# Kernel tuning notes

Hardware: AMD Instinct MI355X
Metric: run time of the kernel (lower is better)

The kernel has to match this reference:

```python
import jax, jax.numpy as jnp
import numpy as np
from jax import lax

D_MODEL = 1024
H = 16
D_K = D_MODEL // H
B = 2
S = 1024


def _conv3x3(x, w, b):
    # x: [B, C_in, S, S], w: [C_out, C_in, 3, 3], b: [C_out]; SAME padding=1
    y = lax.conv_general_dilated(x, w, window_strides=(1, 1),
                                 padding=((1, 1), (1, 1)),
                                 dimension_numbers=("NCHW", "OIHW", "NCHW"))
    return y + b[None, :, None, None]


def setup_inputs() -> dict:
    key = jax.random.key(0)
    ks = jax.random.split(key, 12)
    q = jax.random.normal(ks[0], (B, S, D_MODEL), dtype=jnp.float32)
    k = jax.random.normal(ks[1], (B, S, D_MODEL), dtype=jnp.float32)
    v = jax.random.normal(ks[2], (B, S, D_MODEL), dtype=jnp.float32)
    mask = jax.random.randint(ks[3], (B, S), 0, 2, dtype=jnp.int32)
    prev = jax.random.normal(ks[4], (B, H, S, S), dtype=jnp.float32)
    sc = 1.0 / np.sqrt(D_MODEL)
    Wq = jax.random.normal(ks[5], (D_MODEL, D_MODEL), dtype=jnp.float32) * sc
    Wk = jax.random.normal(ks[6], (D_MODEL, D_MODEL), dtype=jnp.float32) * sc
    Wv = jax.random.normal(ks[7], (D_MODEL, D_MODEL), dtype=jnp.float32) * sc
    Wo = jax.random.normal(ks[8], (D_MODEL, D_MODEL), dtype=jnp.float32) * sc
    csc = 1.0 / np.sqrt(H * 9)
    Wt = jax.random.normal(ks[9], (H, H, 3, 3), dtype=jnp.float32) * csc
    bt = jnp.zeros((H,), dtype=jnp.float32)
    Wa = jax.random.normal(ks[10], (H, 2 * H, 3, 3), dtype=jnp.float32) * csc
    ba = jnp.zeros((H,), dtype=jnp.float32)
    return {"q": q, "k": k, "v": v, "mask": mask,
            "previous_attention_scores": prev,
            "Wq": Wq, "Wk": Wk, "Wv": Wv, "Wo": Wo,
            "Wt": Wt, "bt": bt, "Wa": Wa, "ba": ba}


def reference(q, k, v, mask, previous_attention_scores,
              Wq, Wk, Wv, Wo, Wt, bt, Wa, ba):
    # Linear projections (torch Linear: x @ W.T), reshape to [B, H, S, D_K]
    def split_heads(x):
        return x.reshape(B, S, H, D_K).transpose(0, 2, 1, 3)
    query = split_heads(q @ Wq.T)
    key_ = split_heads(k @ Wk.T)
    value = split_heads(v @ Wv.T)

    # Raw (unscaled) scores: [B, H, S, S]
    M = jnp.einsum("bhsd,bhtd->bhst", query, key_)
    # Transmit conv on previous layer's attention scores (heads = channels)
    Mt = _conv3x3(previous_attention_scores, Wt, bt)
    # Aggregate conv over concatenated [M, Mt]: 2H -> H channels
    Ma = _conv3x3(jnp.concatenate((M, Mt), axis=1), Wa, ba)
    # NOTE: original scales by sqrt(d_model), not sqrt(d_k)
    A = jax.nn.softmax(Ma / jnp.sqrt(jnp.float32(D_MODEL)), axis=-1)
    # NOTE: original applies masked_fill(-1e9) AFTER softmax (faithful)
    A = jnp.where(mask[:, None, None, :] == 0, jnp.float32(-1e9), A)

    ctx = jnp.einsum("bhst,bhtd->bhsd", A, value)  # [B, H, S, D_K]
    ctx = ctx.transpose(0, 2, 1, 3).reshape(B, S, H * D_K)
    out = ctx @ Wo.T
    return out, A
```

## Files before the change

kernel.cpp:

```cpp
#include <hip/hip_runtime.h>

#define B_  2
#define S_  1024
#define H_  16
#define DK_ 64
#define D_  1024

static const size_t BSD  = (size_t)B_ * S_ * D_;
static const size_t BHSS = (size_t)B_ * H_ * S_ * S_;

typedef __attribute__((ext_vector_type(8))) short bf16x8;
typedef __attribute__((ext_vector_type(4))) float floatx4;

__device__ __forceinline__ unsigned short f2bf(float f) {
  unsigned u = __builtin_bit_cast(unsigned, f);
  unsigned r = (u + 0x7FFFu + ((u >> 16) & 1u)) >> 16;
  return (unsigned short)r;
}

__global__ __launch_bounds__(256) void cvt_bf16_kernel(
    const float* __restrict__ src, unsigned short* __restrict__ dst, int n4) {
  int i = (blockIdx.x << 8) + threadIdx.x;
  if (i >= n4) return;
  float4 v = ((const float4*)src)[i];
  ushort4 o;
  o.x = f2bf(v.x); o.y = f2bf(v.y); o.z = f2bf(v.z); o.w = f2bf(v.w);
  ((ushort4*)dst)[i] = o;
}

__global__ __launch_bounds__(256) void gemm_bf16_nt_kernel(
    const unsigned short* __restrict__ A, const unsigned short* __restrict__ Bw,
    void* __restrict__ Cout, int K, int Mcols, int bf16_out,
    const float* __restrict__ corr) {
  __shared__ short As[64 * 40];
  __shared__ short Bs[64 * 40];
  int tid = threadIdx.x;
  int lane = tid & 63, w = tid >> 6;
  int quad = lane >> 4, xn = lane & 15;
  int row0 = blockIdx.y << 6, col0 = blockIdx.x << 6;
  int rw = w & 1, cw = w >> 1;
  int srow = tid >> 2, sk = (tid & 3) << 3;
  const unsigned short* Ap = A + (size_t)(row0 + srow) * K + sk;
  const unsigned short* Bp = Bw + (size_t)(col0 + srow) * K + sk;
  floatx4 acc[2][2] = {};
  for (int k0 = 0; k0 < K; k0 += 32) {
    uint4 av = *(const uint4*)(Ap + k0);
    uint4 bv = *(const uint4*)(Bp + k0);
    *(uint4*)&As[srow * 40 + sk] = av;
    *(uint4*)&Bs[srow * 40 + sk] = bv;
    __syncthreads();
    bf16x8 af[2], bf[2];
#pragma unroll
    for (int rt = 0; rt < 2; ++rt)
      af[rt] = *(const bf16x8*)&As[(rw * 32 + rt * 16 + xn) * 40 + quad * 8];
#pragma unroll
    for (int ct = 0; ct < 2; ++ct)
      bf[ct] = *(const bf16x8*)&Bs[(cw * 32 + ct * 16 + xn) * 40 + quad * 8];
#pragma unroll
    for (int rt = 0; rt < 2; ++rt)
#pragma unroll
      for (int ct = 0; ct < 2; ++ct)
        acc[rt][ct] = __builtin_amdgcn_mfma_f32_16x16x32_bf16(
            af[rt], bf[ct], acc[rt][ct], 0, 0, 0);
    __syncthreads();
  }
#pragma unroll
  for (int rt = 0; rt < 2; ++rt)
#pragma unroll
    for (int ct = 0; ct < 2; ++ct) {
      int colg = col0 + cw * 32 + ct * 16 + xn;
#pragma unroll
      for (int r = 0; r < 4; ++r) {
        int rowg = row0 + rw * 32 + rt * 16 + quad * 4 + r;
        if (bf16_out)
          ((unsigned short*)Cout)[(size_t)rowg * Mcols + colg] = f2bf(acc[rt][ct][r]);
        else {
          float v = acc[rt][ct][r];
          if (corr) v += corr[((rowg >> 10) << 10) + colg];
          ((float*)Cout)[(size_t)rowg * Mcols + colg] = v;
        }
      }
    }
}

__global__ __launch_bounds__(256) void scores_mfma_kernel(
    const unsigned short* __restrict__ Q, const unsigned short* __restrict__ Km,
    unsigned short* __restrict__ Mo) {
  __shared__ short Qs[128 * 72];
  __shared__ short Ks[64 * 72];
  int z = blockIdx.z, b = z >> 4, h = z & 15;
  int col0 = blockIdx.x << 6, row0 = blockIdx.y << 7;
  int tid = threadIdx.x;
  int lane = tid & 63, w = tid >> 6;
  int quad = lane >> 4, xn = lane & 15;
  const unsigned short* Qb = Q + (size_t)b * S_ * D_ + h * DK_;
  const unsigned short* Kb = Km + (size_t)b * S_ * D_ + h * DK_;
  for (int idx = tid; idx < 1024; idx += 256) {
    int r = idx >> 3, k8 = (idx & 7) << 3;
    uint4 v = *(const uint4*)&Qb[(size_t)(row0 + r) * D_ + k8];
    *(uint4*)&Qs[r * 72 + k8] = v;
  }
  for (int idx = tid; idx < 512; idx += 256) {
    int r = idx >> 3, k8 = (idx & 7) << 3;
    uint4 v = *(const uint4*)&Kb[(size_t)(col0 + r) * D_ + k8];
    *(uint4*)&Ks[r * 72 + k8] = v;
  }
  __syncthreads();
  floatx4 acc[2][4] = {};
#pragma unroll
  for (int ks = 0; ks < 2; ++ks) {
    bf16x8 af[2], bf[4];
#pragma unroll
    for (int rt = 0; rt < 2; ++rt)
      af[rt] = *(const bf16x8*)&Qs[(w * 32 + rt * 16 + xn) * 72 + ks * 32 + quad * 8];
#pragma unroll
    for (int ct = 0; ct < 4; ++ct)
      bf[ct] = *(const bf16x8*)&Ks[(ct * 16 + xn) * 72 + ks * 32 + quad * 8];
#pragma unroll
    for (int rt = 0; rt < 2; ++rt)
#pragma unroll
      for (int ct = 0; ct < 4; ++ct)
        acc[rt][ct] = __builtin_amdgcn_mfma_f32_16x16x32_bf16(
            af[rt], bf[ct], acc[rt][ct], 0, 0, 0);
  }
  unsigned short* Mb = Mo + (size_t)z * S_ * S_;
#pragma unroll
  for (int rt = 0; rt < 2; ++rt)
#pragma unroll
    for (int ct = 0; ct < 4; ++ct) {
      int t = col0 + ct * 16 + xn;
#pragma unroll
      for (int r = 0; r < 4; ++r) {
        int s = row0 + w * 32 + rt * 16 + quad * 4 + r;
        Mb[(size_t)s * S_ + t] = f2bf(acc[rt][ct][r]);
      }
    }
}

__global__ __launch_bounds__(256) void repack16b_kernel(
    const unsigned short* __restrict__ src, unsigned short* __restrict__ dst) {
  int x = (blockIdx.x << 8) + threadIdx.x;
  int y = blockIdx.y, b = blockIdx.z;
  const unsigned short* sp = src + ((size_t)b * 16 * S_ + y) * S_ + x;
  unsigned short out[16];
#pragma unroll
  for (int c = 0; c < 16; ++c) out[c] = sp[(size_t)c << 20];
  unsigned short* dp = dst + (((size_t)b * S_ + y) * S_ + x) * 16;
  unsigned wds[8];
#pragma unroll
  for (int i = 0; i < 8; ++i)
    wds[i] = (unsigned)out[2 * i] | ((unsigned)out[2 * i + 1] << 16);
  uint4 v0 = {wds[0], wds[1], wds[2], wds[3]};
  uint4 v1 = {wds[4], wds[5], wds[6], wds[7]};
  *(uint4*)dp = v0;
  *((uint4*)dp + 1) = v1;
}

__global__ __launch_bounds__(256) void repack16_kernel(
    const float* __restrict__ src, unsigned short* __restrict__ dst) {
  int x = (blockIdx.x << 8) + threadIdx.x;
  int y = blockIdx.y, b = blockIdx.z;
  const float* sp = src + ((size_t)b * 16 * S_ + y) * S_ + x;
  unsigned short out[16];
#pragma unroll
  for (int c = 0; c < 16; ++c) out[c] = f2bf(sp[(size_t)c << 20]);
  unsigned short* dp = dst + (((size_t)b * S_ + y) * S_ + x) * 16;
  unsigned wds[8];
#pragma unroll
  for (int i = 0; i < 8; ++i)
    wds[i] = (unsigned)out[2 * i] | ((unsigned)out[2 * i + 1] << 16);
  uint4 v0 = {wds[0], wds[1], wds[2], wds[3]};
  uint4 v1 = {wds[4], wds[5], wds[6], wds[7]};
  *(uint4*)dp = v0;
  *((uint4*)dp + 1) = v1;
}

__global__ __launch_bounds__(256) void conv_t_mfma_kernel(
    const unsigned short* __restrict__ prevT, const float* __restrict__ Wt,
    const float* __restrict__ bt, unsigned short* __restrict__ Mtbf) {
  __shared__ short Xs[10 * 66 * 24];
  int b = blockIdx.z;
  int x0 = blockIdx.x << 6, y0 = blockIdx.y << 3;
  int tid = threadIdx.x;
  int lane = tid & 63, w = tid >> 6;
  int quad = lane >> 4, xn = lane & 15;

  for (int idx = tid; idx < 1320; idx += 256) {
    int y = idx / 132;
    int r = idx - y * 132;
    int px = r >> 1, half = r & 1;
    int gy = y0 + y - 1, gx = x0 + px - 1;
    uint4 val = {0u, 0u, 0u, 0u};
    if ((unsigned)gy < (unsigned)S_ && (unsigned)gx < (unsigned)S_) {
      const unsigned short* sp =
          prevT + (((size_t)b * S_ + gy) * S_ + gx) * 16 + half * 8;
      val = *(const uint4*)sp;
    }
    *(uint4*)&Xs[(y * 66 + px) * 24 + half * 8] = val;
  }

  int m = xn;
  bf16x8 afr[5];
#pragma unroll
  for (int p = 0; p < 5; ++p) {
#pragma unroll
    for (int j = 0; j < 8; ++j) {
      int k = quad * 8 + j;
      int t = 2 * p + (k >> 4);
      float wv = 0.f;
      if (t < 9) wv = Wt[(m * 16 + (k & 15)) * 9 + t];
      afr[p][j] = (short)f2bf(wv);
    }
  }
  int tdy[5], tdx[5];
#pragma unroll
  for (int p = 0; p < 5; ++p) {
    int t = 2 * p + (quad >> 1);
    if (t > 8) t = 8;
    tdy[p] = t / 3;
    tdx[p] = t - tdy[p] * 3;
  }
  float btl[4];
#pragma unroll
  for (int r = 0; r < 4; ++r) btl[r] = bt[quad * 4 + r];

  __syncthreads();

#pragma unroll
  for (int ry = 0; ry < 2; ++ry) {
    int yl = w * 2 + ry;
    int y = y0 + yl;
#pragma unroll
    for (int seg = 0; seg < 4; ++seg) {
      floatx4 acc = {0.f, 0.f, 0.f, 0.f};
#pragma unroll
      for (int p = 0; p < 5; ++p) {
        const short* bp =
            &Xs[((yl + tdy[p]) * 66 + seg * 16 + xn + tdx[p]) * 24 + (quad & 1) * 8];
        bf16x8 bfr = *(const bf16x8*)bp;
        acc = __builtin_amdgcn_mfma_f32_16x16x32_bf16(afr[p], bfr, acc, 0, 0, 0);
      }
      ushort4 pk;
      pk.x = f2bf(acc[0] + btl[0]);
      pk.y = f2bf(acc[1] + btl[1]);
      pk.z = f2bf(acc[2] + btl[2]);
      pk.w = f2bf(acc[3] + btl[3]);
      int gx = x0 + seg * 16 + xn;
      *(ushort4*)&Mtbf[(((size_t)b * S_ + y) * S_ + gx) * 16 + quad * 4] = pk;
    }
  }
}

__global__ __launch_bounds__(256) void conv_a_softmax_kernel(
    const unsigned short* __restrict__ Mbf, const unsigned short* __restrict__ Mtbf,
    const float* __restrict__ Wa, const float* __restrict__ ba,
    const int* __restrict__ mask,
    float* __restrict__ Aout, unsigned short* __restrict__ P0) {
  __shared__ __attribute__((aligned(16))) short Xs[4 * 3 * 34 * 40];
  __shared__ float redm[4][4][4];
  __shared__ float reds[4][4][4];
  int y = ((blockIdx.x & 7) << 7) + (blockIdx.x >> 3);
  int b = blockIdx.y;
  int tid = threadIdx.x;
  int lane = tid & 63, w = tid >> 6;
  int quad = lane >> 4, xn = lane & 15;

  bf16x8 afr[9];
#pragma unroll
  for (int t = 0; t < 9; ++t)
#pragma unroll
    for (int j = 0; j < 8; ++j)
      afr[t][j] = (short)f2bf(Wa[(xn * 32 + quad * 8 + j) * 9 + t]);
  float bal[4];
#pragma unroll
  for (int r = 0; r < 4; ++r) bal[r] = ba[quad * 4 + r];

  short* XsW = &Xs[w * (3 * 34 * 40)];

  int px4 = lane >> 2, part = lane & 3;
  const unsigned short* rowp[3];
  int vy[3];
#pragma unroll
  for (int ry = 0; ry < 3; ++ry) {
    int gy = y + ry - 1;
    vy[ry] = ((unsigned)gy < (unsigned)S_) ? 1 : 0;
    int gyc = vy[ry] ? gy : 0;
    const unsigned short* base = (part < 2) ? Mbf : Mtbf;
    rowp[ry] = base + ((size_t)b * S_ + gyc) * (S_ * 16) + (part & 1) * 8;
  }

  floatx4 acc[8][2] = {};
#pragma unroll
  for (int ci = 0; ci < 8; ++ci) {
    int x0 = (ci << 7) + (w << 5);
#pragma unroll
    for (int ry = 0; ry < 3; ++ry) {
#pragma unroll
      for (int g = 0; g < 3; ++g) {
        if (g < 2 || px4 < 2) {
          int px = (g << 4) + px4;
          int gx = x0 + px - 1;
          uint4 val = {0u, 0u, 0u, 0u};
          if (vy[ry] && (unsigned)gx < (unsigned)S_)
            val = *(const uint4*)(rowp[ry] + (size_t)gx * 16);
          *(uint4*)&XsW[(ry * 34 + px) * 40 + part * 8] = val;
        }
      }
    }
    __builtin_amdgcn_wave_barrier();
#pragma unroll
    for (int sub = 0; sub < 2; ++sub) {
      int sp = (sub << 4) + xn;
      floatx4 a = acc[ci][sub];
#pragma unroll
      for (int t = 0; t < 9; ++t) {
        const int dy = t / 3, dx = t - (t / 3) * 3;
        bf16x8 bfr = *(const bf16x8*)&XsW[(dy * 34 + sp + dx) * 40 + quad * 8];
        a = __builtin_amdgcn_mfma_f32_16x16x32_bf16(afr[t], bfr, a, 0, 0, 0);
      }
      acc[ci][sub] = a;
    }
    __builtin_amdgcn_wave_barrier();
  }

  const float sc = 1.0f / 32.0f;
  float mx[4] = {-3.4e38f, -3.4e38f, -3.4e38f, -3.4e38f};
#pragma unroll
  for (int ci = 0; ci < 8; ++ci)
#pragma unroll
    for (int sub = 0; sub < 2; ++sub)
#pragma unroll
      for (int r = 0; r < 4; ++r) {
        float v = (acc[ci][sub][r] + bal[r]) * sc;
        acc[ci][sub][r] = v;
        mx[r] = fmaxf(mx[r], v);
      }
#pragma unroll
  for (int r = 0; r < 4; ++r) {
    mx[r] = fmaxf(mx[r], __shfl_xor(mx[r], 1));
    mx[r] = fmaxf(mx[r], __shfl_xor(mx[r], 2));
    mx[r] = fmaxf(mx[r], __shfl_xor(mx[r], 4));
    mx[r] = fmaxf(mx[r], __shfl_xor(mx[r], 8));
  }
  if (xn == 0) {
#pragma unroll
    for (int r = 0; r < 4; ++r) redm[w][quad][r] = mx[r];
  }
  __syncthreads();
  float fm[4];
#pragma unroll
  for (int r = 0; r < 4; ++r)
    fm[r] = fmaxf(fmaxf(redm[0][quad][r], redm[1][quad][r]),
                  fmaxf(redm[2][quad][r], redm[3][quad][r]));
  float sm[4] = {0.f, 0.f, 0.f, 0.f};
#pragma unroll
  for (int ci = 0; ci < 8; ++ci)
#pragma unroll
    for (int sub = 0; sub < 2; ++sub)
#pragma unroll
      for (int r = 0; r < 4; ++r) {
        float e = __expf(acc[ci][sub][r] - fm[r]);
        acc[ci][sub][r] = e;
        sm[r] += e;
      }
#pragma unroll
  for (int r = 0; r < 4; ++r) {
    sm[r] += __shfl_xor(sm[r], 1);
    sm[r] += __shfl_xor(sm[r], 2);
    sm[r] += __shfl_xor(sm[r], 4);
    sm[r] += __shfl_xor(sm[r], 8);
  }
  if (xn == 0) {
#pragma unroll
    for (int r = 0; r < 4; ++r) reds[w][quad][r] = sm[r];
  }
  __syncthreads();
  float inv[4];
#pragma unroll
  for (int r = 0; r < 4; ++r)
    inv[r] = 1.0f / (reds[0][quad][r] + reds[1][quad][r] +
                     reds[2][quad][r] + reds[3][quad][r]);

  const int* mb = mask + b * S_;
#pragma unroll
  for (int ci = 0; ci < 8; ++ci)
#pragma unroll
    for (int sub = 0; sub < 2; ++sub) {
      int gx = (ci << 7) + (w << 5) + (sub << 4) + xn;
      int mk = mb[gx];
#pragma unroll
      for (int r = 0; r < 4; ++r) {
        int mo = quad * 4 + r;
        size_t oidx = (((size_t)(b * 16 + mo)) << 20) + ((size_t)y << 10) + gx;
        float p = acc[ci][sub][r] * inv[r];
        Aout[oidx] = mk ? p : -1e9f;
        P0[oidx]  = mk ? f2bf(p) : (unsigned short)0;
      }
    }
}

__global__ __launch_bounds__(256) void vtrans_kernel(
    const float* __restrict__ V, unsigned short* __restrict__ Vt) {
  __shared__ unsigned short Ls[64][68];
  int z = blockIdx.y, b = z >> 4, h = z & 15;
  int t0 = blockIdx.x << 6;
  int tid = threadIdx.x;
  for (int idx = tid; idx < 1024; idx += 256) {
    int t = idx >> 4, d = (idx & 15) << 2;
    float4 v4 = *(const float4*)&V[((size_t)b * S_ + t0 + t) * D_ + h * 64 + d];
    ushort4 u;
    u.x = f2bf(v4.x); u.y = f2bf(v4.y); u.z = f2bf(v4.z); u.w = f2bf(v4.w);
    *(ushort4*)&Ls[t][d] = u;
  }
  __syncthreads();
  for (int idx = tid; idx < 1024; idx += 256) {
    int d = idx >> 4, tc = (idx & 15) << 2;
    ushort4 u;
    u.x = Ls[tc + 0][d]; u.y = Ls[tc + 1][d];
    u.z = Ls[tc + 2][d]; u.w = Ls[tc + 3][d];
    *(ushort4*)&Vt[((size_t)(h * 64 + d)) * 2048 + (size_t)b * S_ + t0 + tc] = u;
  }
}

__global__ __launch_bounds__(256) void colsum_part_kernel(
    const float* __restrict__ V, const int* __restrict__ mask,
    float* __restrict__ cs_part) {
  int b = blockIdx.z, c = blockIdx.y;
  int d = (blockIdx.x << 8) + threadIdx.x;
  const int* mb = mask + b * S_ + c * 32;
  const float* vp = V + ((size_t)b * S_ + c * 32) * D_ + d;
  float s = 0.f;
#pragma unroll
  for (int i = 0; i < 32; ++i) {
    float vv = vp[(size_t)i * D_];
    if (mb[i] == 0) s += vv;
  }
  cs_part[((size_t)b * 32 + c) * D_ + d] = s;
}

__global__ __launch_bounds__(256) void colsum_reduce_kernel(
    const float* __restrict__ cs_part, float* __restrict__ cs) {
  int i = (blockIdx.x << 8) + threadIdx.x;
  int b = i >> 10, d = i & 1023;
  const float* pp = cs_part + ((size_t)b * 32) * D_ + d;
  float s = 0.f;
#pragma unroll
  for (int c = 0; c < 32; ++c) s += pp[(size_t)c * D_];
  cs[i] = s;
}

__global__ __launch_bounds__(256) void corr_kernel(
    const float* __restrict__ cs, const float* __restrict__ Wo,
    float* __restrict__ corr) {
  int b = blockIdx.y;
  int j = (blockIdx.x << 6) + (threadIdx.x >> 2);
  int part = threadIdx.x & 3;
  const float* c = cs + b * D_ + part * 256;
  const float* wr = Wo + (size_t)j * D_ + part * 256;
  float s = 0.f;
  for (int i = 0; i < 256; i += 4) {
    float4 w4 = *(const float4*)&wr[i];
    float4 c4 = *(const float4*)&c[i];
    s = fmaf(w4.x, c4.x, s); s = fmaf(w4.y, c4.y, s);
    s = fmaf(w4.z, c4.z, s); s = fmaf(w4.w, c4.w, s);
  }
  s += __shfl_xor(s, 1);
  s += __shfl_xor(s, 2);
  if (part == 0) corr[b * D_ + j] = -1e9f * s;
}

__global__ __launch_bounds__(256) void ctx_mfma_kernel(
    const unsigned short* __restrict__ P0, const unsigned short* __restrict__ Vt,
    unsigned short* __restrict__ Cbf) {
  __shared__ __attribute__((aligned(16))) short Ps[64 * 72];
  __shared__ __attribute__((aligned(16))) short Vs[64 * 72];
  int z = blockIdx.y, b = z >> 4, h = z & 15;
  int row0 = blockIdx.x << 6;
  int tid = threadIdx.x, lane = tid & 63, w = tid >> 6;
  int quad = lane >> 4, xn = lane & 15;
  const unsigned short* Pb = P0 + (size_t)z * S_ * S_ + (size_t)row0 * S_;
  const unsigned short* Vb = Vt + ((size_t)h * 64) * 2048 + (size_t)b * S_;
  floatx4 acc[4] = {};
  for (int k0 = 0; k0 < S_; k0 += 64) {
    for (int idx = tid; idx < 512; idx += 256) {
      int r = idx >> 3, c = (idx & 7) << 3;
      *(uint4*)&Ps[r * 72 + c] = *(const uint4*)&Pb[(size_t)r * S_ + k0 + c];
    }
    for (int idx = tid; idx < 512; idx += 256) {
      int r = idx >> 3, c = (idx & 7) << 3;
      *(uint4*)&Vs[r * 72 + c] = *(const uint4*)&Vb[(size_t)r * 2048 + k0 + c];
    }
    __syncthreads();
#pragma unroll
    for (int ks = 0; ks < 2; ++ks) {
      bf16x8 af = *(const bf16x8*)&Ps[(w * 16 + xn) * 72 + ks * 32 + quad * 8];
#pragma unroll
      for (int ct = 0; ct < 4; ++ct) {
        bf16x8 bfv = *(const bf16x8*)&Vs[(ct * 16 + xn) * 72 + ks * 32 + quad * 8];
        acc[ct] = __builtin_amdgcn_mfma_f32_16x16x32_bf16(af, bfv, acc[ct], 0, 0, 0);
      }
    }
    __syncthreads();
  }
  unsigned short* Co = Cbf + ((size_t)b * S_) * D_ + h * 64;
#pragma unroll
  for (int ct = 0; ct < 4; ++ct)
#pragma unroll
    for (int r = 0; r < 4; ++r) {
      int s = row0 + w * 16 + quad * 4 + r;
      Co[(size_t)s * D_ + ct * 16 + xn] = f2bf(acc[ct][r]);
    }
}

extern "C" void kernel_launch(void* const* d_in, const int* in_sizes, int n_in,
                              void* d_out, int out_size, void* d_ws, size_t ws_size,
                              hipStream_t stream) {
  const float* q    = (const float*)d_in[0];
  const float* k    = (const float*)d_in[1];
  const float* v    = (const float*)d_in[2];
  const int*   mask = (const int*)d_in[3];
  const float* prev = (const float*)d_in[4];
  const float* Wq   = (const float*)d_in[5];
  const float* Wk   = (const float*)d_in[6];
  const float* Wv   = (const float*)d_in[7];
  const float* Wo   = (const float*)d_in[8];
  const float* Wt   = (const float*)d_in[9];
  const float* bt   = (const float*)d_in[10];
  const float* Wa   = (const float*)d_in[11];
  const float* ba   = (const float*)d_in[12];

  float* out0 = (float*)d_out;
  float* Aout = out0 + BSD;

  char* wsp = (char*)d_ws;
  unsigned short* X1   = (unsigned short*)wsp; wsp += BSD * 2;
  unsigned short* W1   = (unsigned short*)wsp; wsp += (size_t)D_ * D_ * 2;
  unsigned short* Qb   = (unsigned short*)wsp; wsp += BSD * 2;
  unsigned short* Kb   = (unsigned short*)wsp; wsp += BSD * 2;
  float* Vb            = (float*)wsp;          wsp += BSD * 4;
  unsigned short* Vtb  = (unsigned short*)wsp; wsp += BSD * 2;
  unsigned short* ctx1 = (unsigned short*)wsp; wsp += BSD * 2;
  float* cs            = (float*)wsp;          wsp += (size_t)B_ * D_ * 4;
  float* corrb         = (float*)wsp;          wsp += (size_t)B_ * D_ * 4;
  float* cs_part       = (float*)wsp;          wsp += (size_t)B_ * 32 * D_ * 4;
  unsigned short* Mp   = (unsigned short*)wsp; wsp += BHSS * 2;
  unsigned short* Mbf  = (unsigned short*)wsp; wsp += BHSS * 2;
  unsigned short* Mtbf = (unsigned short*)wsp; wsp += BHSS * 2;
  unsigned short* prevT = Mp;
  unsigned short* P0    = Mp;

  dim3 blk(256);
  int n4x = (int)(BSD / 4);
  int n4w = (D_ * D_) / 4;
  dim3 gX((n4x + 255) / 256), gW((n4w + 255) / 256);
  dim3 gProjB(D_ / 64, (B_ * S_) / 64);

  hipLaunchKernelGGL(cvt_bf16_kernel, gW, blk, 0, stream, Wq, W1, n4w);
  hipLaunchKernelGGL(cvt_bf16_kernel, gX, blk, 0, stream, q, X1, n4x);
  hipLaunchKernelGGL(gemm_bf16_nt_kernel, gProjB, blk, 0, stream, X1, W1,
                     (void*)Qb, D_, D_, 1, (const float*)nullptr);
  hipLaunchKernelGGL(cvt_bf16_kernel, gW, blk, 0, stream, Wk, W1, n4w);
  hipLaunchKernelGGL(cvt_bf16_kernel, gX, blk, 0, stream, k, X1, n4x);
  hipLaunchKernelGGL(gemm_bf16_nt_kernel, gProjB, blk, 0, stream, X1, W1,
                     (void*)Kb, D_, D_, 1, (const float*)nullptr);
  hipLaunchKernelGGL(cvt_bf16_kernel, gW, blk, 0, stream, Wv, W1, n4w);
  hipLaunchKernelGGL(cvt_bf16_kernel, gX, blk, 0, stream, v, X1, n4x);
  hipLaunchKernelGGL(gemm_bf16_nt_kernel, gProjB, blk, 0, stream, X1, W1,
                     (void*)Vb, D_, D_, 0, (const float*)nullptr);
  hipLaunchKernelGGL(cvt_bf16_kernel, gW, blk, 0, stream, Wo, W1, n4w);

  hipLaunchKernelGGL(vtrans_kernel, dim3(S_ / 64, B_ * H_), blk, 0, stream, Vb, Vtb);
  hipLaunchKernelGGL(colsum_part_kernel, dim3(D_ / 256, 32, B_), blk, 0, stream,
                     Vb, mask, cs_part);
  hipLaunchKernelGGL(colsum_reduce_kernel, dim3((B_ * D_) / 256), blk, 0, stream,
                     cs_part, cs);
  hipLaunchKernelGGL(corr_kernel, dim3(D_ / 64, B_), blk, 0, stream, cs, Wo, corrb);

  dim3 gSc(S_ / 64, S_ / 128, B_ * H_);
  hipLaunchKernelGGL(scores_mfma_kernel, gSc, blk, 0, stream, Qb, Kb, Mp);

  dim3 gRep(S_ / 256, S_, B_);
  hipLaunchKernelGGL(repack16b_kernel, gRep, blk, 0, stream, Mp, Mbf);

  hipLaunchKernelGGL(repack16_kernel, gRep, blk, 0, stream, prev, prevT);

  dim3 gConv(S_ / 64, S_ / 8, B_);
  hipLaunchKernelGGL(conv_t_mfma_kernel, gConv, blk, 0, stream, prevT, Wt, bt, Mtbf);

  hipLaunchKernelGGL(conv_a_softmax_kernel, dim3(S_, B_), blk, 0, stream,
                     Mbf, Mtbf, Wa, ba, mask, Aout, P0);

  hipLaunchKernelGGL(ctx_mfma_kernel, dim3(S_ / 64, B_ * H_), blk, 0, stream,
                     P0, Vtb, ctx1);

  dim3 gProj(D_ / 64, (B_ * S_) / 64);
  hipLaunchKernelGGL(gemm_bf16_nt_kernel, gProj, blk, 0, stream, ctx1, W1,
                     (void*)out0, D_, D_, 0, (const float*)corrb);
}
```

Baseline: 675.9 us.

## Prefetch next conv tile into registers and repack LDS layout per channel-quad

In the aggregate-conv+softmax kernel, global loads for the next 32-column chunk are issued into registers before the MFMA work on the current chunk, software-pipelining global latency behind compute. The LDS staging layout changes from pixel-major with 40-short padding to a [row][channel-quad][pixel] layout with 8-short rows. This shrinks LDS per block and changes bank access patterns. Load index math is precomputed once per thread. The cost is extra registers for seven uint4 prefetch buffers plus precomputed pointers, which may reduce occupancy.

```diff
diff --git a/kernel.cpp b/kernel.cpp
--- a/kernel.cpp
+++ b/kernel.cpp
@@ -256,7 +256,7 @@
     const float* __restrict__ Wa, const float* __restrict__ ba,
     const int* __restrict__ mask,
     float* __restrict__ Aout, unsigned short* __restrict__ P0) {
-  __shared__ __attribute__((aligned(16))) short Xs[4 * 3 * 34 * 40];
+  __shared__ __attribute__((aligned(16))) short Xs[4 * 3264];
   __shared__ float redm[4][4][4];
   __shared__ float reds[4][4][4];
   int y = ((blockIdx.x & 7) << 7) + (blockIdx.x >> 3);
@@ -275,39 +275,63 @@
 #pragma unroll
   for (int r = 0; r < 4; ++r) bal[r] = ba[quad * 4 + r];
 
-  short* XsW = &Xs[w * (3 * 34 * 40)];
-
-  int px4 = lane >> 2, part = lane & 3;
-  const unsigned short* rowp[3];
-  int vy[3];
-#pragma unroll
-  for (int ry = 0; ry < 3; ++ry) {
+  short* XsW = &Xs[w * 3264];
+
+  const unsigned short* s_base[7];
+  int s_pxo[7], s_lds[7], s_vy[7];
+#pragma unroll
+  for (int it = 0; it < 7; ++it) {
+    int s = it * 64 + lane;
+    int ry = (s >= 272) ? 2 : ((s >= 136) ? 1 : 0);
+    int rem = s - ry * 136;
+    int px = rem >> 2, part = rem & 3;
     int gy = y + ry - 1;
-    vy[ry] = ((unsigned)gy < (unsigned)S_) ? 1 : 0;
-    int gyc = vy[ry] ? gy : 0;
+    int vyy = ((unsigned)gy < (unsigned)S_) ? 1 : 0;
+    int gyc = vyy ? gy : 0;
     const unsigned short* base = (part < 2) ? Mbf : Mtbf;
-    rowp[ry] = base + ((size_t)b * S_ + gyc) * (S_ * 16) + (part & 1) * 8;
+    s_base[it] = base + ((size_t)b * S_ + gyc) * (S_ * 16) + (part & 1) * 8
+                 + (size_t)(px - 1) * 16;
+    s_vy[it]  = vyy;
+    s_pxo[it] = px - 1;
+    s_lds[it] = ((ry * 4 + part) * 34 + px) * 8;
+  }
+
+  uint4 ld[7];
+  {
+    int x0 = (w << 5);
+#pragma unroll
+    for (int it = 0; it < 7; ++it) {
+      uint4 val = {0u, 0u, 0u, 0u};
+      if (it < 6 || lane < 24) {
+        int gx = x0 + s_pxo[it];
+        if (s_vy[it] && (unsigned)gx < (unsigned)S_)
+          val = *(const uint4*)(s_base[it] + (size_t)x0 * 16);
+      }
+      ld[it] = val;
+    }
   }
 
   floatx4 acc[8][2] = {};
 #pragma unroll
   for (int ci = 0; ci < 8; ++ci) {
-    int x0 = (ci << 7) + (w << 5);
-#pragma unroll
-    for (int ry = 0; ry < 3; ++ry) {
-#pragma unroll
-      for (int g = 0; g < 3; ++g) {
-        if (g < 2 || px4 < 2) {
-          int px = (g << 4) + px4;
-          int gx = x0 + px - 1;
-          uint4 val = {0u, 0u, 0u, 0u};
-          if (vy[ry] && (unsigned)gx < (unsigned)S_)
-            val = *(const uint4*)(rowp[ry] + (size_t)gx * 16);
-          *(uint4*)&XsW[(ry * 34 + px) * 40 + part * 8] = val;
+#pragma unroll
+    for (int it = 0; it < 7; ++it)
+      if (it < 6 || lane < 24)
+        *(uint4*)&XsW[s_lds[it]] = ld[it];
+    __builtin_amdgcn_wave_barrier();
+    if (ci < 7) {
+      int x0n = ((ci + 1) << 7) + (w << 5);
+#pragma unroll
+      for (int it = 0; it < 7; ++it) {
+        uint4 val = {0u, 0u, 0u, 0u};
+        if (it < 6 || lane < 24) {
+          int gx = x0n + s_pxo[it];
+          if (s_vy[it] && (unsigned)gx < (unsigned)S_)
+            val = *(const uint4*)(s_base[it] + (size_t)x0n * 16);
         }
-      }
-    }
-    __builtin_amdgcn_wave_barrier();
+        ld[it] = val;
+      }
+    }
 #pragma unroll
     for (int sub = 0; sub < 2; ++sub) {
       int sp = (sub << 4) + xn;
@@ -315,7 +339,7 @@
 #pragma unroll
       for (int t = 0; t < 9; ++t) {
         const int dy = t / 3, dx = t - (t / 3) * 3;
-        bf16x8 bfr = *(const bf16x8*)&XsW[(dy * 34 + sp + dx) * 40 + quad * 8];
+        bf16x8 bfr = *(const bf16x8*)&XsW[((dy * 4 + quad) * 34 + sp + dx) * 8];
         a = __builtin_amdgcn_mfma_f32_16x16x32_bf16(afr[t], bfr, a, 0, 0, 0);
       }
       acc[ci][sub] = a;
```

Result: faster. 659.9 us (-2.4%).
